# Optimization experiments

Hardware: AMD Instinct MI355X
Metric: run time of the kernel (lower is better)

Reference implementation:

```python
import jax, jax.numpy as jnp
import numpy as np

VOCAB = 50000
D_EMB = 300
N_BINS = 11
B, LQ, LD = 64, 32, 1024
MU = np.array([1.0, 0.9, 0.7, 0.5, 0.3, 0.1, -0.1, -0.3, -0.5, -0.7, -0.9], dtype=np.float32)
SIGMA = np.array([1e-3] + [0.1] * 10, dtype=np.float32)


def setup_inputs() -> dict:
    key = jax.random.key(0)
    ks = jax.random.split(key, 8)
    inputs_q = jax.random.randint(ks[0], (B, LQ), 0, VOCAB, dtype=jnp.int64 if jax.config.jax_enable_x64 else jnp.int32)
    inputs_d = jax.random.randint(ks[1], (B, LD), 0, VOCAB, dtype=jnp.int64 if jax.config.jax_enable_x64 else jnp.int32)
    mask_q = jnp.ones((B, LQ), dtype=jnp.float32)
    mask_d = jnp.ones((B, LD), dtype=jnp.float32)
    word_emb = jax.random.normal(ks[2], (VOCAB, D_EMB), dtype=jnp.float32) * 0.1
    attn_table = jax.random.uniform(ks[3], (VOCAB, 1), dtype=jnp.float32)  # frozen IDF embedding
    idf_w = jax.random.normal(ks[4], (1, 1), dtype=jnp.float32)
    idf_b = jnp.zeros((1,), dtype=jnp.float32)
    dense_w = jax.random.normal(ks[5], (1, N_BINS), dtype=jnp.float32) * 0.1
    dense_b = jnp.zeros((1,), dtype=jnp.float32)
    return {
        'inputs_q': inputs_q, 'inputs_d': inputs_d,
        'mask_q': mask_q, 'mask_d': mask_d,
        'word_emb': word_emb, 'attn_table': attn_table,
        'idf_w': idf_w, 'idf_b': idf_b,
        'dense_w': dense_w, 'dense_b': dense_b,
    }


def _l2_normalize(x, eps=1e-12):
    # matches F.normalize(x, 2, dim=-1): x / max(||x||, eps)
    n = jnp.sqrt(jnp.sum(x * x, axis=-1, keepdims=True))
    return x / jnp.maximum(n, eps)


def reference(inputs_q, inputs_d, mask_q, mask_d, word_emb, attn_table,
              idf_w, idf_b, dense_w, dense_b):
    mu = jnp.asarray(MU)        # [K]
    sigma = jnp.asarray(SIGMA)  # [K]
    # idf attention on query tokens: Linear(1,1) on frozen embedding lookup
    attn_q = attn_table[inputs_q] * idf_w[0, 0] + idf_b[0]          # [B,Lq,1]
    q_embed = _l2_normalize(word_emb[inputs_q])                      # [B,Lq,E]
    d_embed = _l2_normalize(word_emb[inputs_d])                      # [B,Ld,E]
    sim = jnp.einsum('bqe,bde->bqd', q_embed, d_embed)               # [B,Lq,Ld]
    # RBF soft-histogram over n_bins kernels, doc tokens masked
    rbf = jnp.exp(-((sim[..., None] - mu) ** 2) / (sigma ** 2) / 2)  # [B,Lq,Ld,K]
    pooling_sum = jnp.einsum('bqdk,bd->bqk', rbf, mask_d)            # [B,Lq,K]
    wq = mask_q[..., None] * attn_q                                   # [B,Lq,1]
    log_pool = jnp.log(jnp.clip(pooling_sum, 1e-10)) * wq * 0.01     # [B,Lq,K]
    log_pooling_sum = jnp.sum(log_pool, axis=1)                      # [B,K]
    out = jnp.tanh(log_pooling_sum @ dense_w.T + dense_b)            # [B,1]
    return out[:, 0]                                                 # [B]
```

## Files before the change

### kernel.cpp

```cpp
#include <hip/hip_runtime.h>
#include <math.h>

#define VOCAB   50000
#define D_EMB   300
#define NBINS   11
#define BATCH   64
#define LQ      32
#define LD      1024
#define NCHUNK  8
#define NSTEP   10
#define FRAG_SHORTS (NSTEP * 512)

typedef __attribute__((ext_vector_type(8))) short short8;
typedef __attribute__((ext_vector_type(4))) float floatx4;

__constant__ float c_mu[NBINS]  = {1.0f, 0.9f, 0.7f, 0.5f, 0.3f, 0.1f,
                                   -0.1f, -0.3f, -0.5f, -0.7f, -0.9f};
__constant__ float c_is2[NBINS] = {500000.0f, 50.f, 50.f, 50.f, 50.f, 50.f,
                                   50.f, 50.f, 50.f, 50.f, 50.f};

static __device__ __forceinline__ unsigned short f32_bf16(float f) {
  unsigned u = __float_as_uint(f);
  u += 0x7FFFu + ((u >> 16) & 1u);
  return (unsigned short)(u >> 16);
}
static __device__ __forceinline__ float bf16_f32(unsigned short h) {
  return __uint_as_float(((unsigned)h) << 16);
}

static __device__ __forceinline__ float gather_convert(
    const float* __restrict__ emb_row, short8* __restrict__ frag,
    int khi)
{
  const float4* emb4 = (const float4*)emb_row;
  float p = 0.f;
#pragma unroll
  for (int s = 0; s < NSTEP; ++s) {
    const int k0 = 32 * s + 8 * khi;
    float4 fa = make_float4(0.f, 0.f, 0.f, 0.f);
    float4 fb = make_float4(0.f, 0.f, 0.f, 0.f);
    if (k0 < D_EMB)     fa = emb4[k0 >> 2];
    if (k0 + 4 < D_EMB) fb = emb4[(k0 >> 2) + 1];
    unsigned short h[8];
    h[0] = f32_bf16(fa.x); h[1] = f32_bf16(fa.y);
    h[2] = f32_bf16(fa.z); h[3] = f32_bf16(fa.w);
    h[4] = f32_bf16(fb.x); h[5] = f32_bf16(fb.y);
    h[6] = f32_bf16(fb.z); h[7] = f32_bf16(fb.w);
    short8 v;
#pragma unroll
    for (int j = 0; j < 8; ++j) {
      const float x = bf16_f32(h[j]);
      p += x * x;
      v[j] = (short)h[j];
    }
    frag[s] = v;
  }
  return p;
}

__global__ __launch_bounds__(256, 2) void knrm_fused(
    const int* __restrict__ inputs_q, const int* __restrict__ inputs_d,
    const float* __restrict__ mask_d, const float* __restrict__ word_emb,
    float* __restrict__ partial)
{
  const int b    = blockIdx.y;
  const int j    = blockIdx.x;
  const int tid  = threadIdx.x;
  const int wid  = tid >> 6;
  const int lane = tid & 63;
  const int khi  = lane >> 4;
  const int rl   = lane & 15;

  __shared__ __align__(16) short Alds[2 * FRAG_SHORTS];
  __shared__ float invq_lds[LQ];
  __shared__ float red[4][2][16][NBINS];

  const int dbase = b * LD + j * 128 + 32 * wid;

  const int td0 = inputs_d[dbase + rl];
  const int td1 = inputs_d[dbase + 16 + rl];
  short8 bf0[NSTEP], bf1[NSTEP];
  float pb0 = gather_convert(word_emb + (size_t)td0 * D_EMB, bf0, khi);
  float pb1 = gather_convert(word_emb + (size_t)td1 * D_EMB, bf1, khi);
  pb0 += __shfl_xor(pb0, 16); pb0 += __shfl_xor(pb0, 32);
  pb1 += __shfl_xor(pb1, 16); pb1 += __shfl_xor(pb1, 32);
  const float id0 = 1.f / fmaxf(sqrtf(pb0), 1e-12f);
  const float id1 = 1.f / fmaxf(sqrtf(pb1), 1e-12f);

  if (wid < 2) {
    const int tq = inputs_q[b * LQ + 16 * wid + rl];
    short8 af[NSTEP];
    float pa = gather_convert(word_emb + (size_t)tq * D_EMB, af, khi);
    short8* dst = (short8*)(Alds + wid * FRAG_SHORTS);
#pragma unroll
    for (int s = 0; s < NSTEP; ++s) dst[s * 64 + lane] = af[s];
    pa += __shfl_xor(pa, 16); pa += __shfl_xor(pa, 32);
    if (lane < 16) invq_lds[16 * wid + lane] = 1.f / fmaxf(sqrtf(pa), 1e-12f);
  }
  __syncthreads();

  floatx4 acc[2][2] = {{{0.f,0.f,0.f,0.f},{0.f,0.f,0.f,0.f}},
                       {{0.f,0.f,0.f,0.f},{0.f,0.f,0.f,0.f}}};
#pragma unroll
  for (int s = 0; s < NSTEP; ++s) {
    const short8 a0 = *(const short8*)(Alds + s * 512 + lane * 8);
    const short8 a1 = *(const short8*)(Alds + FRAG_SHORTS + s * 512 + lane * 8);
    acc[0][0] = __builtin_amdgcn_mfma_f32_16x16x32_bf16(a0, bf0[s], acc[0][0], 0, 0, 0);
    acc[0][1] = __builtin_amdgcn_mfma_f32_16x16x32_bf16(a0, bf1[s], acc[0][1], 0, 0, 0);
    acc[1][0] = __builtin_amdgcn_mfma_f32_16x16x32_bf16(a1, bf0[s], acc[1][0], 0, 0, 0);
    acc[1][1] = __builtin_amdgcn_mfma_f32_16x16x32_bf16(a1, bf1[s], acc[1][1], 0, 0, 0);
  }

  const float md0 = mask_d[dbase + rl];
  const float md1 = mask_d[dbase + 16 + rl];
#pragma unroll
  for (int qt = 0; qt < 2; ++qt) {
    float ps[4][NBINS];
#pragma unroll
    for (int r = 0; r < 4; ++r) {
      const float iq = invq_lds[16 * qt + 4 * khi + r];
      const float s0 = acc[qt][0][r] * iq * id0;
      const float s1 = acc[qt][1][r] * iq * id1;
#pragma unroll
      for (int k = 0; k < NBINS; ++k) {
        const float d0 = s0 - c_mu[k];
        const float d1 = s1 - c_mu[k];
        ps[r][k] = md0 * __expf(-d0 * d0 * c_is2[k])
                 + md1 * __expf(-d1 * d1 * c_is2[k]);
      }
    }
#pragma unroll
    for (int off = 1; off < 16; off <<= 1)
#pragma unroll
      for (int r = 0; r < 4; ++r)
#pragma unroll
        for (int k = 0; k < NBINS; ++k)
          ps[r][k] += __shfl_xor(ps[r][k], off);
    if (rl == 0)
#pragma unroll
      for (int r = 0; r < 4; ++r)
#pragma unroll
        for (int k = 0; k < NBINS; ++k)
          red[wid][qt][4 * khi + r][k] = ps[r][k];
  }
  __syncthreads();

  for (int v = tid; v < LQ * NBINS; v += 256) {
    const int q = v / NBINS, k = v % NBINS;
    const int qt = q >> 4, qr = q & 15;
    const float sv = red[0][qt][qr][k] + red[1][qt][qr][k]
                   + red[2][qt][qr][k] + red[3][qt][qr][k];
    partial[((size_t)(b * LQ + q) * NBINS + k) * NCHUNK + j] = sv;
  }
}

__global__ __launch_bounds__(128) void knrm_finalize(
    const float* __restrict__ partial, const int* __restrict__ inputs_q,
    const float* __restrict__ mask_q, const float* __restrict__ attn_table,
    const float* __restrict__ idf_w, const float* __restrict__ idf_b,
    const float* __restrict__ dense_w, const float* __restrict__ dense_b,
    float* __restrict__ out)
{
  const int b   = blockIdx.x;
  const int tid = threadIdx.x;
  __shared__ float pool[LQ][NBINS];
  __shared__ float wq_s[LQ];
  __shared__ float lps[NBINS];

  for (int v = tid; v < LQ * NBINS; v += 128) {
    const int q = v / NBINS, k = v % NBINS;
    const float* p = partial + ((size_t)(b * LQ + q) * NBINS + k) * NCHUNK;
    float s = 0.f;
#pragma unroll
    for (int t = 0; t < NCHUNK; ++t) s += p[t];
    pool[q][k] = logf(fmaxf(s, 1e-10f));
  }
  if (tid < LQ) {
    const int tok = inputs_q[b * LQ + tid];
    wq_s[tid] = mask_q[b * LQ + tid] * (attn_table[tok] * idf_w[0] + idf_b[0]);
  }
  __syncthreads();
  if (tid < NBINS) {
    float s = 0.f;
    for (int q = 0; q < LQ; ++q) s += pool[q][tid] * wq_s[q];
    lps[tid] = 0.01f * s;
  }
  __syncthreads();
  if (tid == 0) {
    float z = dense_b[0];
    for (int k = 0; k < NBINS; ++k) z += lps[k] * dense_w[k];
    out[b] = tanhf(z);
  }
}

extern "C" void kernel_launch(void* const* d_in, const int* in_sizes, int n_in,
                              void* d_out, int out_size, void* d_ws, size_t ws_size,
                              hipStream_t stream) {
  const int*   inputs_q  = (const int*)d_in[0];
  const int*   inputs_d  = (const int*)d_in[1];
  const float* mask_q    = (const float*)d_in[2];
  const float* mask_d    = (const float*)d_in[3];
  const float* word_emb  = (const float*)d_in[4];
  const float* attn_tab  = (const float*)d_in[5];
  const float* idf_w     = (const float*)d_in[6];
  const float* idf_b     = (const float*)d_in[7];
  const float* dense_w   = (const float*)d_in[8];
  const float* dense_b   = (const float*)d_in[9];
  float* out     = (float*)d_out;
  float* partial = (float*)d_ws;

  dim3 grid(NCHUNK, BATCH);
  knrm_fused<<<grid, 256, 0, stream>>>(inputs_q, inputs_d, mask_d, word_emb, partial);
  knrm_finalize<<<BATCH, 128, 0, stream>>>(partial, inputs_q, mask_q, attn_tab,
                                           idf_w, idf_b, dense_w, dense_b, out);
}
```

Measured before the change: 141.9 us.

## Halve per-wave doc tile, double chunks, raise occupancy to four blocks per CU

Each wave now handles 16 document tokens instead of 32, so the grid doubles to 16 chunks per batch and launch bounds request 4 blocks per SM. Query fragments are written straight to LDS during conversion rather than staged in registers, and the document gather is issued after the query gather so the two can overlap. This cuts register pressure to allow more resident waves for latency hiding on the random embedding gathers. In exchange, query embeddings are gathered and converted twice as many times in total, and the shuffle reductions run per 16 tokens, which doubles that overhead per token.

```diff
diff --git a/kernel.cpp b/kernel.cpp
--- a/kernel.cpp
+++ b/kernel.cpp
@@ -7,7 +7,7 @@
 #define BATCH   64
 #define LQ      32
 #define LD      1024
-#define NCHUNK  8
+#define NCHUNK  16
 #define NSTEP   10
 #define FRAG_SHORTS (NSTEP * 512)
 
@@ -29,8 +29,7 @@
 }
 
 static __device__ __forceinline__ float gather_convert(
-    const float* __restrict__ emb_row, short8* __restrict__ frag,
-    int khi)
+    const float* __restrict__ emb_row, short8* __restrict__ frag, int khi)
 {
   const float4* emb4 = (const float4*)emb_row;
   float p = 0.f;
@@ -58,7 +57,37 @@
   return p;
 }
 
-__global__ __launch_bounds__(256, 2) void knrm_fused(
+static __device__ __forceinline__ float gather_convert_lds(
+    const float* __restrict__ emb_row, short* __restrict__ region,
+    int khi, int lane)
+{
+  const float4* emb4 = (const float4*)emb_row;
+  float p = 0.f;
+#pragma unroll
+  for (int s = 0; s < NSTEP; ++s) {
+    const int k0 = 32 * s + 8 * khi;
+    float4 fa = make_float4(0.f, 0.f, 0.f, 0.f);
+    float4 fb = make_float4(0.f, 0.f, 0.f, 0.f);
+    if (k0 < D_EMB)     fa = emb4[k0 >> 2];
+    if (k0 + 4 < D_EMB) fb = emb4[(k0 >> 2) + 1];
+    unsigned short h[8];
+    h[0] = f32_bf16(fa.x); h[1] = f32_bf16(fa.y);
+    h[2] = f32_bf16(fa.z); h[3] = f32_bf16(fa.w);
+    h[4] = f32_bf16(fb.x); h[5] = f32_bf16(fb.y);
+    h[6] = f32_bf16(fb.z); h[7] = f32_bf16(fb.w);
+    short8 v;
+#pragma unroll
+    for (int j = 0; j < 8; ++j) {
+      const float x = bf16_f32(h[j]);
+      p += x * x;
+      v[j] = (short)h[j];
+    }
+    *(short8*)(region + s * 512 + lane * 8) = v;
+  }
+  return p;
+}
+
+__global__ __launch_bounds__(256, 4) void knrm_fused(
     const int* __restrict__ inputs_q, const int* __restrict__ inputs_d,
     const float* __restrict__ mask_d, const float* __restrict__ word_emb,
     float* __restrict__ partial)
@@ -75,58 +104,44 @@
   __shared__ float invq_lds[LQ];
   __shared__ float red[4][2][16][NBINS];
 
-  const int dbase = b * LD + j * 128 + 32 * wid;
-
-  const int td0 = inputs_d[dbase + rl];
-  const int td1 = inputs_d[dbase + 16 + rl];
-  short8 bf0[NSTEP], bf1[NSTEP];
-  float pb0 = gather_convert(word_emb + (size_t)td0 * D_EMB, bf0, khi);
-  float pb1 = gather_convert(word_emb + (size_t)td1 * D_EMB, bf1, khi);
-  pb0 += __shfl_xor(pb0, 16); pb0 += __shfl_xor(pb0, 32);
-  pb1 += __shfl_xor(pb1, 16); pb1 += __shfl_xor(pb1, 32);
-  const float id0 = 1.f / fmaxf(sqrtf(pb0), 1e-12f);
-  const float id1 = 1.f / fmaxf(sqrtf(pb1), 1e-12f);
+  const int dbase = b * LD + j * 64 + 16 * wid;
 
   if (wid < 2) {
     const int tq = inputs_q[b * LQ + 16 * wid + rl];
-    short8 af[NSTEP];
-    float pa = gather_convert(word_emb + (size_t)tq * D_EMB, af, khi);
-    short8* dst = (short8*)(Alds + wid * FRAG_SHORTS);
-#pragma unroll
-    for (int s = 0; s < NSTEP; ++s) dst[s * 64 + lane] = af[s];
+    float pa = gather_convert_lds(word_emb + (size_t)tq * D_EMB,
+                                  Alds + wid * FRAG_SHORTS, khi, lane);
     pa += __shfl_xor(pa, 16); pa += __shfl_xor(pa, 32);
     if (lane < 16) invq_lds[16 * wid + lane] = 1.f / fmaxf(sqrtf(pa), 1e-12f);
   }
-  __syncthreads();
-
-  floatx4 acc[2][2] = {{{0.f,0.f,0.f,0.f},{0.f,0.f,0.f,0.f}},
-                       {{0.f,0.f,0.f,0.f},{0.f,0.f,0.f,0.f}}};
+
+  const int td = inputs_d[dbase + rl];
+  short8 bf[NSTEP];
+  float pb = gather_convert(word_emb + (size_t)td * D_EMB, bf, khi);
+  pb += __shfl_xor(pb, 16); pb += __shfl_xor(pb, 32);
+  const float id = 1.f / fmaxf(sqrtf(pb), 1e-12f);
+  __syncthreads();
+
+  floatx4 acc[2] = {{0.f,0.f,0.f,0.f},{0.f,0.f,0.f,0.f}};
 #pragma unroll
   for (int s = 0; s < NSTEP; ++s) {
     const short8 a0 = *(const short8*)(Alds + s * 512 + lane * 8);
     const short8 a1 = *(const short8*)(Alds + FRAG_SHORTS + s * 512 + lane * 8);
-    acc[0][0] = __builtin_amdgcn_mfma_f32_16x16x32_bf16(a0, bf0[s], acc[0][0], 0, 0, 0);
-    acc[0][1] = __builtin_amdgcn_mfma_f32_16x16x32_bf16(a0, bf1[s], acc[0][1], 0, 0, 0);
-    acc[1][0] = __builtin_amdgcn_mfma_f32_16x16x32_bf16(a1, bf0[s], acc[1][0], 0, 0, 0);
-    acc[1][1] = __builtin_amdgcn_mfma_f32_16x16x32_bf16(a1, bf1[s], acc[1][1], 0, 0, 0);
-  }
-
-  const float md0 = mask_d[dbase + rl];
-  const float md1 = mask_d[dbase + 16 + rl];
+    acc[0] = __builtin_amdgcn_mfma_f32_16x16x32_bf16(a0, bf[s], acc[0], 0, 0, 0);
+    acc[1] = __builtin_amdgcn_mfma_f32_16x16x32_bf16(a1, bf[s], acc[1], 0, 0, 0);
+  }
+
+  const float md = mask_d[dbase + rl];
 #pragma unroll
   for (int qt = 0; qt < 2; ++qt) {
     float ps[4][NBINS];
 #pragma unroll
     for (int r = 0; r < 4; ++r) {
       const float iq = invq_lds[16 * qt + 4 * khi + r];
-      const float s0 = acc[qt][0][r] * iq * id0;
-      const float s1 = acc[qt][1][r] * iq * id1;
+      const float sv = acc[qt][r] * iq * id;
 #pragma unroll
       for (int k = 0; k < NBINS; ++k) {
-        const float d0 = s0 - c_mu[k];
-        const float d1 = s1 - c_mu[k];
-        ps[r][k] = md0 * __expf(-d0 * d0 * c_is2[k])
-                 + md1 * __expf(-d1 * d1 * c_is2[k]);
+        const float d = sv - c_mu[k];
+        ps[r][k] = md * __expf(-d * d * c_is2[k]);
       }
     }
 #pragma unroll
```

Measured after the change: 139.2 us. No clear change (-1.9%).
